# Kernel optimization log

Measured on AMD Instinct MI355X. Metric: run time of the kernel, lower is better.

The kernel has to match this reference:

```python
import jax, jax.numpy as jnp
import numpy as np

H = 128
N_USER, N_PC, N_URL = 100000, 20000, 50000
E_UP, E_UU = 250000, 500000
NUM_LAYERS = 2


def _sage(x_src, x_dst, src_idx, dst_idx, n_dst, Wl, bl, Wr):
    # PyG SAGEConv (aggr='mean', root_weight=True, lin_r bias=False):
    # out = lin_l(mean_j x_src[j]) + lin_r(x_dst)
    msg = x_src[src_idx]                                   # [E, H] gather
    agg = jax.ops.segment_sum(msg, dst_idx, num_segments=n_dst)
    cnt = jax.ops.segment_sum(jnp.ones((src_idx.shape[0], 1), x_src.dtype),
                              dst_idx, num_segments=n_dst)
    mean = agg / jnp.maximum(cnt, 1.0)
    return mean @ Wl + bl + x_dst @ Wr


def setup_inputs() -> dict:
    key = jax.random.key(0)
    ks = jax.random.split(key, 24)
    s = 0.05
    inp = {
        'x_user': jax.random.normal(ks[0], (N_USER, 6), jnp.float32),
        'x_pc': jax.random.normal(ks[1], (N_PC, 4), jnp.float32),
        'x_url': jax.random.normal(ks[2], (N_URL, 3), jnp.float32),
        'edge_up_src': jax.random.randint(ks[3], (E_UP,), 0, N_USER, jnp.int32),
        'edge_up_dst': jax.random.randint(ks[4], (E_UP,), 0, N_PC, jnp.int32),
        'edge_uu_src': jax.random.randint(ks[5], (E_UU,), 0, N_USER, jnp.int32),
        'edge_uu_dst': jax.random.randint(ks[6], (E_UU,), 0, N_URL, jnp.int32),
        # input projections
        'Wu': jax.random.normal(ks[7], (6, H), jnp.float32) * s,
        'bu': jnp.zeros((H,), jnp.float32),
        'Wp': jax.random.normal(ks[8], (4, H), jnp.float32) * s,
        'bp': jnp.zeros((H,), jnp.float32),
        'Wr_feat': jax.random.normal(ks[9], (3, H), jnp.float32) * s,
        'br_feat': jnp.zeros((H,), jnp.float32),
        # SAGEConv params, stacked over layers [L, H, H]
        'Wl_pc': jax.random.normal(ks[10], (NUM_LAYERS, H, H), jnp.float32) * s,
        'bl_pc': jnp.zeros((NUM_LAYERS, H), jnp.float32),
        'Wr_pc': jax.random.normal(ks[11], (NUM_LAYERS, H, H), jnp.float32) * s,
        'Wl_url': jax.random.normal(ks[12], (NUM_LAYERS, H, H), jnp.float32) * s,
        'bl_url': jnp.zeros((NUM_LAYERS, H), jnp.float32),
        'Wr_url': jax.random.normal(ks[13], (NUM_LAYERS, H, H), jnp.float32) * s,
        # context aggregation + classifier
        'Wctx': jax.random.normal(ks[14], (3 * H, H), jnp.float32) * s,
        'bctx': jnp.zeros((H,), jnp.float32),
        'Wc1': jax.random.normal(ks[15], (H, H // 2), jnp.float32) * s,
        'bc1': jnp.zeros((H // 2,), jnp.float32),
        'Wc2': jax.random.normal(ks[16], (H // 2, 2), jnp.float32) * s,
        'bc2': jnp.zeros((2,), jnp.float32),
    }
    return inp


def reference(x_user, x_pc, x_url,
              edge_up_src, edge_up_dst, edge_uu_src, edge_uu_dst,
              Wu, bu, Wp, bp, Wr_feat, br_feat,
              Wl_pc, bl_pc, Wr_pc, Wl_url, bl_url, Wr_url,
              Wctx, bctx, Wc1, bc1, Wc2, bc2):
    user = x_user @ Wu + bu          # [N_USER, H] (never updated by convs)
    pc = x_pc @ Wp + bp              # [N_PC, H]
    url = x_url @ Wr_feat + br_feat  # [N_URL, H]

    for i in range(NUM_LAYERS):
        pc_new = _sage(user, pc, edge_up_src, edge_up_dst, pc.shape[0],
                       Wl_pc[i], bl_pc[i], Wr_pc[i])
        url_new = _sage(user, url, edge_uu_src, edge_uu_dst, url.shape[0],
                        Wl_url[i], bl_url[i], Wr_url[i])
        if i == 0:
            pc = jax.nn.relu(pc_new)
            url = jax.nn.relu(url_new)
        else:
            pc = jax.nn.relu(pc_new + pc)
            url = jax.nn.relu(url_new + url)

    # aggregate_resource_context: scatter-add of resource embeddings into users
    pc_ctx = jax.ops.segment_sum(pc[edge_up_dst], edge_up_src, num_segments=user.shape[0])
    url_ctx = jax.ops.segment_sum(url[edge_uu_dst], edge_uu_src, num_segments=user.shape[0])
    combined = jnp.concatenate([user, pc_ctx, url_ctx], axis=1)   # [N_USER, 3H]
    enriched = combined @ Wctx + bctx

    # classifier (dropout inactive at inference)
    h = jax.nn.relu(enriched @ Wc1 + bc1)
    return h @ Wc2 + bc2
```

## Files before the change

### kernel.cpp

```cpp
#include <hip/hip_runtime.h>

typedef unsigned short u16;
typedef short short8_t __attribute__((ext_vector_type(8)));
typedef float floatx4 __attribute__((ext_vector_type(4)));

static constexpr int N_USER_C = 100000;
static constexpr int N_PC_C   = 20000;
static constexpr int N_URL_C  = 50000;
static constexpr int E_UP_C   = 250000;
static constexpr int E_UU_C   = 500000;

static constexpr int S_UPD = 48;
static constexpr int S_UUD = 40;
static constexpr int S_SRC = 24;

__device__ __forceinline__ float bf2f(u16 h) {
    return __uint_as_float(((unsigned)h) << 16);
}
__device__ __forceinline__ u16 f2bf(float f) {
    unsigned u = __float_as_uint(f);
    u += 0x7fffu + ((u >> 16) & 1u);
    return (u16)(u >> 16);
}

struct PFArgs {
    const float* wsrc[12];
    u16* wdst;
    const float *Xu, *Wu, *bu, *Xp, *Wp, *bp, *Xr, *Wr, *br;
    u16 *ou, *op, *orr;
    const int *up_src, *up_dst, *uu_src, *uu_dst;
    int *cnt_up_dst, *cnt_uu_dst, *cnt_up_src, *cnt_uu_src;
    int *val_up_dst, *val_uu_dst;
    u16 *val_up_src, *val_uu_src;
};
__global__ __launch_bounds__(256) void prepfill_kernel(PFArgs a)
{
    int b = blockIdx.x, tid = threadIdx.x;
    if (b < 1960) {
        const int range = b & 7;
        const int ebase = (b >> 3) * 2048 + tid;
#pragma unroll
        for (int i = 0; i < 8; ++i) {
            int e = ebase + i * 256;
            if (e < E_UP_C) {
                int s = __builtin_nontemporal_load(a.up_src + e);
                int d = __builtin_nontemporal_load(a.up_dst + e);
                if (d / 2500 == range) {
                    int p = atomicAdd(&a.cnt_up_dst[d], 1);
                    if (p < S_UPD) a.val_up_dst[d * S_UPD + p] = s;
                }
                if (s / 12500 == range) {
                    int p = atomicAdd(&a.cnt_up_src[s], 1);
                    if (p < S_SRC) a.val_up_src[s * S_SRC + p] = (u16)d;
                }
            }
            if (e < E_UU_C) {
                int s = __builtin_nontemporal_load(a.uu_src + e);
                int d = __builtin_nontemporal_load(a.uu_dst + e);
                if (d / 6250 == range) {
                    int p = atomicAdd(&a.cnt_uu_dst[d], 1);
                    if (p < S_UUD) a.val_uu_dst[d * S_UUD + p] = s;
                }
                if (s / 12500 == range) {
                    int p = atomicAdd(&a.cnt_uu_src[s], 1);
                    if (p < S_SRC) a.val_uu_src[s * S_SRC + p] = (u16)d;
                }
            }
        }
    } else if (b < 1960 + 768) {
        int idx = (b - 1960) * 256 + tid;
        int m = idx >> 14, e = idx & 16383;
        int n = e >> 7, k = e & 127;
        int Nm = (m == 11) ? 64 : 128;
        u16 v = 0;
        if (n < Nm) v = f2bf(a.wsrc[m][k * Nm + n]);
        a.wdst[(size_t)m * 16384 + n * 128 + k] = v;
    } else {
        int idx = (b - 1960 - 768) * 256 + tid;
        const float* X; const float* W; const float* bi; u16* o; int K;
        if (idx < 1600000)       { X = a.Xu; W = a.Wu; bi = a.bu; o = a.ou; K = 6; }
        else if (idx < 1920000)  { idx -= 1600000; X = a.Xp; W = a.Wp; bi = a.bp; o = a.op; K = 4; }
        else                     { idx -= 1920000; X = a.Xr; W = a.Wr; bi = a.br; o = a.orr; K = 3; }
        int r = idx >> 4, c0 = (idx & 15) * 8;
        float acc[8];
        {
            const float4 b0 = *(const float4*)(bi + c0);
            const float4 b1 = *(const float4*)(bi + c0 + 4);
            acc[0] = b0.x; acc[1] = b0.y; acc[2] = b0.z; acc[3] = b0.w;
            acc[4] = b1.x; acc[5] = b1.y; acc[6] = b1.z; acc[7] = b1.w;
        }
        for (int k = 0; k < K; ++k) {
            float xk = X[(size_t)r * K + k];
            const float4 w0 = *(const float4*)(W + k * 128 + c0);
            const float4 w1 = *(const float4*)(W + k * 128 + c0 + 4);
            acc[0] += xk * w0.x; acc[1] += xk * w0.y; acc[2] += xk * w0.z; acc[3] += xk * w0.w;
            acc[4] += xk * w1.x; acc[5] += xk * w1.y; acc[6] += xk * w1.z; acc[7] += xk * w1.w;
        }
        uint4 pk;
        pk.x = (unsigned)f2bf(acc[0]) | ((unsigned)f2bf(acc[1]) << 16);
        pk.y = (unsigned)f2bf(acc[2]) | ((unsigned)f2bf(acc[3]) << 16);
        pk.z = (unsigned)f2bf(acc[4]) | ((unsigned)f2bf(acc[5]) << 16);
        pk.w = (unsigned)f2bf(acc[6]) | ((unsigned)f2bf(acc[7]) << 16);
        *(uint4*)(o + (size_t)r * 128 + c0) = pk;
    }
}

__device__ __forceinline__ void gm_row(
    const u16* __restrict__ feat, const int* __restrict__ cnt,
    const int* __restrict__ vals, int stride, u16* __restrict__ outp, int row, int lane)
{
    int deg = cnt[row];
    deg = __builtin_amdgcn_readfirstlane(deg);
    int n = deg < stride ? deg : stride;
    const int* vp = vals + row * stride;
    float a0 = 0.f, a1 = 0.f, b0 = 0.f, b1 = 0.f;
    float c0 = 0.f, c1 = 0.f, d0 = 0.f, d1 = 0.f;
    int j = 0;
    for (; j + 4 <= n; j += 4) {
        int i0 = __builtin_nontemporal_load(vp + j);
        int i1 = __builtin_nontemporal_load(vp + j + 1);
        int i2 = __builtin_nontemporal_load(vp + j + 2);
        int i3 = __builtin_nontemporal_load(vp + j + 3);
        unsigned u0 = *(const unsigned*)(feat + (size_t)i0 * 128 + lane * 2);
        unsigned u1 = *(const unsigned*)(feat + (size_t)i1 * 128 + lane * 2);
        unsigned u2 = *(const unsigned*)(feat + (size_t)i2 * 128 + lane * 2);
        unsigned u3 = *(const unsigned*)(feat + (size_t)i3 * 128 + lane * 2);
        a0 += bf2f((u16)(u0 & 0xffff)); a1 += bf2f((u16)(u0 >> 16));
        b0 += bf2f((u16)(u1 & 0xffff)); b1 += bf2f((u16)(u1 >> 16));
        c0 += bf2f((u16)(u2 & 0xffff)); c1 += bf2f((u16)(u2 >> 16));
        d0 += bf2f((u16)(u3 & 0xffff)); d1 += bf2f((u16)(u3 >> 16));
    }
    for (; j < n; ++j) {
        int i0 = __builtin_nontemporal_load(vp + j);
        unsigned u0 = *(const unsigned*)(feat + (size_t)i0 * 128 + lane * 2);
        a0 += bf2f((u16)(u0 & 0xffff)); a1 += bf2f((u16)(u0 >> 16));
    }
    float ax = (a0 + b0) + (c0 + d0), ay = (a1 + b1) + (c1 + d1);
    float inv = 1.0f / fmaxf((float)deg, 1.0f);
    unsigned o = (unsigned)f2bf(ax * inv) | ((unsigned)f2bf(ay * inv) << 16);
    *(unsigned*)(outp + (size_t)row * 128 + lane * 2) = o;
}

__global__ __launch_bounds__(256) void gather_mean2_kernel(
    const u16* __restrict__ feat,
    const int* __restrict__ cnt_pc, const int* __restrict__ val_pc, u16* __restrict__ out_pc,
    const int* __restrict__ cnt_url, const int* __restrict__ val_url, u16* __restrict__ out_url)
{
    int b = blockIdx.x;
    int lane = threadIdx.x & 63, w = threadIdx.x >> 6;
    if (b < 5000) gm_row(feat, cnt_pc, val_pc, S_UPD, out_pc, b * 4 + w, lane);
    else          gm_row(feat, cnt_url, val_url, S_UUD, out_url, (b - 5000) * 4 + w, lane);
}

__device__ __forceinline__ unsigned ctx_ld(int t, int n0, const u16* __restrict__ vu,
    const u16* __restrict__ vr,
    const u16* __restrict__ pcW, const u16* __restrict__ urlW, int lane)
{
    bool isup = t < n0;
    const u16* vp = isup ? (vu + t) : (vr + (t - n0));
    int idx = __builtin_nontemporal_load(vp);
    const u16* base = isup ? pcW : urlW;
    return *(const unsigned*)(base + (size_t)idx * 128 + lane * 2);
}

__global__ __launch_bounds__(256) void ctx_gather_kernel(
    u16* __restrict__ enr,
    const int* __restrict__ cnt_up, const u16* __restrict__ val_up, const u16* __restrict__ pcW,
    const int* __restrict__ cnt_uu, const u16* __restrict__ val_uu, const u16* __restrict__ urlW,
    int M)
{
    int row = blockIdx.x * 4 + (threadIdx.x >> 6);
    if (row >= M) return;
    int lane = threadIdx.x & 63;
    int n0 = cnt_up[row], n1 = cnt_uu[row];
    n0 = __builtin_amdgcn_readfirstlane(n0); n1 = __builtin_amdgcn_readfirstlane(n1);
    n0 = n0 < S_SRC ? n0 : S_SRC; n1 = n1 < S_SRC ? n1 : S_SRC;
    int total = n0 + n1;
    const u16* vu = val_up + row * S_SRC;
    const u16* vr = val_uu + row * S_SRC;

    unsigned eu = *(const unsigned*)(enr + (size_t)row * 128 + lane * 2);
    float a0 = bf2f((u16)(eu & 0xffff)), a1 = bf2f((u16)(eu >> 16));
    float b0 = 0.f, b1 = 0.f, c0 = 0.f, c1 = 0.f, d0 = 0.f, d1 = 0.f;

    int t = 0;
    for (; t + 4 <= total; t += 4) {
        unsigned u0 = ctx_ld(t + 0, n0, vu, vr, pcW, urlW, lane);
        unsigned u1 = ctx_ld(t + 1, n0, vu, vr, pcW, urlW, lane);
        unsigned u2 = ctx_ld(t + 2, n0, vu, vr, pcW, urlW, lane);
        unsigned u3 = ctx_ld(t + 3, n0, vu, vr, pcW, urlW, lane);
        a0 += bf2f((u16)(u0 & 0xffff)); a1 += bf2f((u16)(u0 >> 16));
        b0 += bf2f((u16)(u1 & 0xffff)); b1 += bf2f((u16)(u1 >> 16));
        c0 += bf2f((u16)(u2 & 0xffff)); c1 += bf2f((u16)(u2 >> 16));
        d0 += bf2f((u16)(u3 & 0xffff)); d1 += bf2f((u16)(u3 >> 16));
    }
    for (; t < total; ++t) {
        unsigned u0 = ctx_ld(t, n0, vu, vr, pcW, urlW, lane);
        a0 += bf2f((u16)(u0 & 0xffff)); a1 += bf2f((u16)(u0 >> 16));
    }
    float ax = (a0 + b0) + (c0 + d0), ay = (a1 + b1) + (c1 + d1);
    unsigned o = (unsigned)f2bf(ax) | ((unsigned)f2bf(ay) << 16);
    *(unsigned*)(enr + (size_t)row * 128 + lane * 2) = o;
}

struct FSeg {
    const u16 *mean, *x0;
    const u16 *Wl0, *Wr0, *Wl1, *Wr1, *Wc;
    const float *b0, *b1;
    u16* out; int M; int bstart; int mode;
};
struct FArgs { FSeg s[3]; };

__global__ __launch_bounds__(256) void gemm_fused_kernel(FArgs fa)
{
    constexpr int XP = 136;
    __shared__ u16 Ws[2][128 * 40];
    __shared__ u16 Xs[128 * XP];

    int si = 0;
    if ((int)blockIdx.x >= fa.s[1].bstart) si = 1;
    if ((int)blockIdx.x >= fa.s[2].bstart) si = 2;
    FSeg sg = fa.s[si];
    const int bb = blockIdx.x - sg.bstart;

    const int tid = threadIdx.x;
    const int wave = tid >> 6, lane = tid & 63;
    const int m = lane & 15, kq = lane >> 4;
    const int rloc = wave * 32;
    const int rbase = bb * 128 + rloc;
    const int sn = tid >> 1, spart = tid & 1;

    floatx4 acc[2][8];

    auto zeroAcc = [&]() {
#pragma unroll
        for (int mt = 0; mt < 2; ++mt)
#pragma unroll
            for (int nt = 0; nt < 8; ++nt) acc[mt][nt] = (floatx4)0.0f;
    };
    auto stageW = [&](const u16* Wt, int kc, int buf) {
        *(short8_t*)&Ws[buf][sn * 40 + spart * 16] =
            *(const short8_t*)(Wt + (size_t)sn * 128 + kc + spart * 16);
        *(short8_t*)&Ws[buf][sn * 40 + spart * 16 + 8] =
            *(const short8_t*)(Wt + (size_t)sn * 128 + kc + spart * 16 + 8);
    };
    auto loadAg = [&](const u16* A, int kc, int mt) -> short8_t {
        int row = rbase + mt * 16 + m; row = row < sg.M ? row : sg.M - 1;
        return *(const short8_t*)(A + (size_t)row * 128 + kc + kq * 8);
    };
    auto loadAs = [&](int kc, int mt) -> short8_t {
        return *(const short8_t*)&Xs[(rloc + mt * 16 + m) * XP + kc + kq * 8];
    };
    auto mfmaChunk = [&](short8_t a0, short8_t a1, int buf) {
#pragma unroll
        for (int nt = 0; nt < 8; ++nt) {
            short8_t b = *(const short8_t*)&Ws[buf][(nt * 16 + m) * 40 + kq * 8];
            acc[0][nt] = __builtin_amdgcn_mfma_f32_16x16x32_bf16(a0, b, acc[0][nt], 0, 0, 0);
            acc[1][nt] = __builtin_amdgcn_mfma_f32_16x16x32_bf16(a1, b, acc[1][nt], 0, 0, 0);
        }
    };
    auto passDual = [&](const u16* W1, const u16* A1g, const u16* W2, const u16* A2g, bool a2lds) {
        zeroAcc();
        stageW(W1, 0, 0);
        short8_t an0 = loadAg(A1g, 0, 0), an1 = loadAg(A1g, 0, 1);
        __syncthreads();
        for (int c = 0; c < 8; ++c) {
            int c1 = c + 1;
            if (c1 < 8) {
                int kc1 = (c1 & 3) * 32;
                stageW(c1 < 4 ? W1 : W2, kc1, c1 & 1);
            }
            short8_t a0 = an0, a1 = an1;
            if (c1 < 8) {
                int kc1 = (c1 & 3) * 32;
                if (c1 < 4)     { an0 = loadAg(A1g, kc1, 0); an1 = loadAg(A1g, kc1, 1); }
                else if (a2lds) { an0 = loadAs(kc1, 0);      an1 = loadAs(kc1, 1); }
                else            { an0 = loadAg(A2g, kc1, 0); an1 = loadAg(A2g, kc1, 1); }
            }
            mfmaChunk(a0, a1, c & 1);
            __syncthreads();
        }
    };
    auto passSingle = [&](const u16* W1, const u16* A1g, bool lds) {
        zeroAcc();
        stageW(W1, 0, 0);
        short8_t an0, an1;
        if (lds) { an0 = loadAs(0, 0); an1 = loadAs(0, 1); }
        else     { an0 = loadAg(A1g, 0, 0); an1 = loadAg(A1g, 0, 1); }
        __syncthreads();
        for (int c = 0; c < 4; ++c) {
            int c1 = c + 1;
            if (c1 < 4) stageW(W1, c1 * 32, c1 & 1);
            short8_t a0 = an0, a1 = an1;
            if (c1 < 4) {
                if (lds) { an0 = loadAs(c1 * 32, 0); an1 = loadAs(c1 * 32, 1); }
                else     { an0 = loadAg(A1g, c1 * 32, 0); an1 = loadAg(A1g, c1 * 32, 1); }
            }
            mfmaChunk(a0, a1, c & 1);
            __syncthreads();
        }
    };
    auto epilogueToLds = [&](const float* bias, bool addRes) {
#pragma unroll
        for (int nt = 0; nt < 8; ++nt) {
            int col = nt * 16 + m;
            float bv = bias[col];
#pragma unroll
            for (int mt = 0; mt < 2; ++mt)
#pragma unroll
                for (int r = 0; r < 4; ++r) {
                    int lrow = rloc + mt * 16 + kq * 4 + r;
                    float v = acc[mt][nt][r] + bv;
                    if (addRes) v += bf2f(Xs[lrow * XP + col]);
                    Xs[lrow * XP + col] = f2bf(fmaxf(v, 0.f));
                }
        }
    };
    auto epilogueToGlobal = [&](const float* bias, u16* outp) {
#pragma unroll
        for (int nt = 0; nt < 8; ++nt) {
            int col = nt * 16 + m;
            float bv = bias ? bias[col] : 0.0f;
#pragma unroll
            for (int mt = 0; mt < 2; ++mt)
#pragma unroll
                for (int r = 0; r < 4; ++r) {
                    int row = rbase + mt * 16 + kq * 4 + r;
                    if (row < sg.M) outp[(size_t)row * 128 + col] = f2bf(acc[mt][nt][r] + bv);
                }
        }
    };

    if (sg.mode == 0) {
        passDual(sg.Wl0, sg.mean, sg.Wr0, sg.x0, false);
        epilogueToLds(sg.b0, false);
        passDual(sg.Wl1, sg.mean, sg.Wr1, nullptr, true);
        epilogueToLds(sg.b1, true);
        passSingle(sg.Wc, nullptr, true);
        epilogueToGlobal(nullptr, sg.out);
    } else {
        passSingle(sg.Wl0, sg.mean, false);
        epilogueToGlobal(sg.b0, sg.out);
    }
}

__global__ __launch_bounds__(256) void gemm_final_kernel(
    const u16* __restrict__ A1, const u16* __restrict__ Wt1,
    const float* __restrict__ bc1, const float* __restrict__ Wc2,
    const float* __restrict__ bc2, float* __restrict__ out, int M)
{
    constexpr int NT = 4;
    constexpr int PER_ROW = 4;
    constexpr int CHUNK = 8;
    constexpr int NC = 4;

    __shared__ u16 Ws[64 * 40];

    const int tid = threadIdx.x;
    const int wave = tid >> 6, lane = tid & 63;
    const int m = lane & 15, kq = lane >> 4;
    const int rbase = blockIdx.x * 128 + wave * 32;
    const int sn = tid / PER_ROW, spart = tid % PER_ROW;

    floatx4 acc[2][NT];
#pragma unroll
    for (int mt = 0; mt < 2; ++mt)
#pragma unroll
        for (int nt = 0; nt < NT; ++nt) acc[mt][nt] = (floatx4)0.0f;

    short8_t a_next[2];
#pragma unroll
    for (int mt = 0; mt < 2; ++mt) {
        int row = rbase + mt * 16 + m; row = row < M ? row : M - 1;
        a_next[mt] = *(const short8_t*)(A1 + (size_t)row * 128 + kq * 8);
    }

    for (int c = 0; c < NC; ++c) {
        __syncthreads();
        {
            short8_t v = *(const short8_t*)(Wt1 + (size_t)sn * 128 + c * 32 + spart * CHUNK);
            *(short8_t*)&Ws[sn * 40 + spart * CHUNK] = v;
        }
        short8_t a_cur[2] = { a_next[0], a_next[1] };
        __syncthreads();
        if (c + 1 < NC) {
            int kc1 = (c + 1) * 32;
#pragma unroll
            for (int mt = 0; mt < 2; ++mt) {
                int row = rbase + mt * 16 + m; row = row < M ? row : M - 1;
                a_next[mt] = *(const short8_t*)(A1 + (size_t)row * 128 + kc1 + kq * 8);
            }
        }
#pragma unroll
        for (int nt = 0; nt < NT; ++nt) {
            short8_t b = *(const short8_t*)&Ws[(nt * 16 + m) * 40 + kq * 8];
            acc[0][nt] = __builtin_amdgcn_mfma_f32_16x16x32_bf16(a_cur[0], b, acc[0][nt], 0, 0, 0);
            acc[1][nt] = __builtin_amdgcn_mfma_f32_16x16x32_bf16(a_cur[1], b, acc[1][nt], 0, 0, 0);
        }
    }

    float w0v[NT], w1v[NT], bv[NT];
#pragma unroll
    for (int nt = 0; nt < NT; ++nt) {
        int col = nt * 16 + m;
        w0v[nt] = Wc2[col * 2 + 0];
        w1v[nt] = Wc2[col * 2 + 1];
        bv[nt]  = bc1[col];
    }
    float b20 = bc2[0], b21 = bc2[1];

#pragma unroll
    for (int mt = 0; mt < 2; ++mt) {
#pragma unroll
        for (int r = 0; r < 4; ++r) {
            float o0 = 0.f, o1 = 0.f;
#pragma unroll
            for (int nt = 0; nt < NT; ++nt) {
                float v = acc[mt][nt][r] + bv[nt];
                v = fmaxf(v, 0.f);
                o0 += v * w0v[nt];
                o1 += v * w1v[nt];
            }
#pragma unroll
            for (int off = 1; off < 16; off <<= 1) {
                o0 += __shfl_xor(o0, off, 64);
                o1 += __shfl_xor(o1, off, 64);
            }
            if (m == 0) {
                int row = rbase + mt * 16 + kq * 4 + r;
                if (row < M) {
                    out[(size_t)row * 2 + 0] = o0 + b20;
                    out[(size_t)row * 2 + 1] = o1 + b21;
                }
            }
        }
    }
}

extern "C" void kernel_launch(void* const* d_in, const int* in_sizes, int n_in,
                              void* d_out, int out_size, void* d_ws, size_t ws_size,
                              hipStream_t stream)
{
    const float* x_user  = (const float*)d_in[0];
    const float* x_pc    = (const float*)d_in[1];
    const float* x_url   = (const float*)d_in[2];
    const int* e_up_src  = (const int*)d_in[3];
    const int* e_up_dst  = (const int*)d_in[4];
    const int* e_uu_src  = (const int*)d_in[5];
    const int* e_uu_dst  = (const int*)d_in[6];
    const float* Wu      = (const float*)d_in[7];
    const float* bu      = (const float*)d_in[8];
    const float* Wp      = (const float*)d_in[9];
    const float* bp      = (const float*)d_in[10];
    const float* Wr_feat = (const float*)d_in[11];
    const float* br_feat = (const float*)d_in[12];
    const float* Wl_pc   = (const float*)d_in[13];
    const float* bl_pc   = (const float*)d_in[14];
    const float* Wr_pc   = (const float*)d_in[15];
    const float* Wl_url  = (const float*)d_in[16];
    const float* bl_url  = (const float*)d_in[17];
    const float* Wr_url  = (const float*)d_in[18];
    const float* Wctx    = (const float*)d_in[19];
    const float* bctx    = (const float*)d_in[20];
    const float* Wc1     = (const float*)d_in[21];
    const float* bc1     = (const float*)d_in[22];
    const float* Wc2     = (const float*)d_in[23];
    const float* bc2     = (const float*)d_in[24];
    float* out = (float*)d_out;

    char* wsb = (char*)d_ws;
    u16* user_bf  = (u16*)(wsb);
    u16* enr      = (u16*)(wsb + 4ull *  6400000);
    u16* mean_pc  = (u16*)(wsb + 4ull * 12800000);
    u16* mean_url = (u16*)(wsb + 4ull * 14080000);
    u16* pc_a     = (u16*)(wsb + 4ull * 17280000);
    u16* pc_b     = (u16*)(wsb + 4ull * 18560000);
    u16* url_a    = (u16*)(wsb + 4ull * 19840000);
    u16* url_b    = (u16*)(wsb + 4ull * 23040000);
    u16* Wt       = (u16*)(wsb + 4ull * 26240000);
    int* cnts     = (int*)(wsb + 4ull * 26340000);
    int* up_dst_val = (int*)(wsb + 4ull * 26610000);
    int* uu_dst_val = (int*)(wsb + 4ull * 27570000);
    u16* up_src_val = (u16*)(wsb + 4ull * 29570000);
    u16* uu_src_val = (u16*)(wsb + 4ull * 30770000);

    int* cnt_up_dst = cnts + 0;
    int* cnt_uu_dst = cnts + 20000;
    int* cnt_up_src = cnts + 70000;
    int* cnt_uu_src = cnts + 170000;

    const int T = 256;

    hipMemsetAsync(cnts, 0, 270000ull * 4, stream);

    PFArgs pf;
    pf.wsrc[0] = Wl_pc;               pf.wsrc[1] = Wr_pc;
    pf.wsrc[2] = Wl_pc + 128 * 128;   pf.wsrc[3] = Wr_pc + 128 * 128;
    pf.wsrc[4] = Wl_url;              pf.wsrc[5] = Wr_url;
    pf.wsrc[6] = Wl_url + 128 * 128;  pf.wsrc[7] = Wr_url + 128 * 128;
    pf.wsrc[8] = Wctx;                pf.wsrc[9] = Wctx + 128 * 128;
    pf.wsrc[10] = Wctx + 256 * 128;   pf.wsrc[11] = Wc1;
    pf.wdst = Wt;
    pf.Xu = x_user; pf.Wu = Wu;      pf.bu = bu;      pf.ou = user_bf;
    pf.Xp = x_pc;   pf.Wp = Wp;      pf.bp = bp;      pf.op = pc_a;
    pf.Xr = x_url;  pf.Wr = Wr_feat; pf.br = br_feat; pf.orr = url_a;
    pf.up_src = e_up_src; pf.up_dst = e_up_dst;
    pf.uu_src = e_uu_src; pf.uu_dst = e_uu_dst;
    pf.cnt_up_dst = cnt_up_dst; pf.cnt_uu_dst = cnt_uu_dst;
    pf.cnt_up_src = cnt_up_src; pf.cnt_uu_src = cnt_uu_src;
    pf.val_up_dst = up_dst_val; pf.val_uu_dst = uu_dst_val;
    pf.val_up_src = up_src_val; pf.val_uu_src = uu_src_val;
    prepfill_kernel<<<1960 + 768 + 10625, T, 0, stream>>>(pf);

    gather_mean2_kernel<<<5000 + 12500, T, 0, stream>>>(
        user_bf, cnt_up_dst, up_dst_val, mean_pc, cnt_uu_dst, uu_dst_val, mean_url);

    FArgs fg;
    fg.s[0] = { mean_pc,  pc_a,  Wt + 0 * 16384, Wt + 1 * 16384, Wt + 2 * 16384, Wt + 3 * 16384,
                Wt + 9 * 16384,  bl_pc,  bl_pc + 128,  pc_b,  N_PC_C,   0,   0 };
    fg.s[1] = { mean_url, url_a, Wt + 4 * 16384, Wt + 5 * 16384, Wt + 6 * 16384, Wt + 7 * 16384,
                Wt + 10 * 16384, bl_url, bl_url + 128, url_b, N_URL_C,  157, 0 };
    fg.s[2] = { user_bf,  nullptr, Wt + 8 * 16384, nullptr, nullptr, nullptr,
                nullptr,         bctx,   nullptr,      enr,   N_USER_C, 548, 1 };
    gemm_fused_kernel<<<548 + 782, T, 0, stream>>>(fg);

    ctx_gather_kernel<<<(N_USER_C + 3) / 4, T, 0, stream>>>(
        enr, cnt_up_src, up_src_val, pc_b, cnt_uu_src, uu_src_val, url_b, N_USER_C);

    gemm_final_kernel<<<(N_USER_C + 127) / 128, T, 0, stream>>>(
        enr, Wt + 11 * 16384, bc1, Wc2, bc2, out, N_USER_C);
}
```

Before: 353.0 us.

## Fuse user ctx GEMM into gather kernel and ctx gather into final classifier

Moves the user-side Wctx projection GEMM out of the fused GEMM launch into the mean-gather launch as extra blocks, so the chain kernel only handles pc/url layers. Merges the context gather with the classifier GEMM: each block gathers 64 rows into LDS, then runs the Wc1 MFMA and the Wc2 reduction in place. This drops the enr round-trip and one launch. In exchange the final kernel stages the whole Wc1 into 64-row LDS tiles, and the gather runs serially per wave over 16 rows, which may reduce memory-level parallelism.

New measurement: 433.1 us. 22.7% more time.

```diff
diff --git a/kernel.cpp b/kernel.cpp
--- a/kernel.cpp
+++ b/kernel.cpp
@@ -141,85 +141,90 @@
     *(unsigned*)(outp + (size_t)row * 128 + lane * 2) = o;
 }
 
-__global__ __launch_bounds__(256) void gather_mean2_kernel(
+__global__ __launch_bounds__(256) void mean_ctx_kernel(
     const u16* __restrict__ feat,
     const int* __restrict__ cnt_pc, const int* __restrict__ val_pc, u16* __restrict__ out_pc,
-    const int* __restrict__ cnt_url, const int* __restrict__ val_url, u16* __restrict__ out_url)
+    const int* __restrict__ cnt_url, const int* __restrict__ val_url, u16* __restrict__ out_url,
+    const u16* __restrict__ Wctx_t, const float* __restrict__ bctx, u16* __restrict__ enr)
 {
-    int b = blockIdx.x;
-    int lane = threadIdx.x & 63, w = threadIdx.x >> 6;
-    if (b < 5000) gm_row(feat, cnt_pc, val_pc, S_UPD, out_pc, b * 4 + w, lane);
-    else          gm_row(feat, cnt_url, val_url, S_UUD, out_url, (b - 5000) * 4 + w, lane);
-}
-
-__device__ __forceinline__ unsigned ctx_ld(int t, int n0, const u16* __restrict__ vu,
-    const u16* __restrict__ vr,
-    const u16* __restrict__ pcW, const u16* __restrict__ urlW, int lane)
-{
-    bool isup = t < n0;
-    const u16* vp = isup ? (vu + t) : (vr + (t - n0));
-    int idx = __builtin_nontemporal_load(vp);
-    const u16* base = isup ? pcW : urlW;
-    return *(const unsigned*)(base + (size_t)idx * 128 + lane * 2);
-}
-
-__global__ __launch_bounds__(256) void ctx_gather_kernel(
-    u16* __restrict__ enr,
-    const int* __restrict__ cnt_up, const u16* __restrict__ val_up, const u16* __restrict__ pcW,
-    const int* __restrict__ cnt_uu, const u16* __restrict__ val_uu, const u16* __restrict__ urlW,
-    int M)
-{
-    int row = blockIdx.x * 4 + (threadIdx.x >> 6);
-    if (row >= M) return;
-    int lane = threadIdx.x & 63;
-    int n0 = cnt_up[row], n1 = cnt_uu[row];
-    n0 = __builtin_amdgcn_readfirstlane(n0); n1 = __builtin_amdgcn_readfirstlane(n1);
-    n0 = n0 < S_SRC ? n0 : S_SRC; n1 = n1 < S_SRC ? n1 : S_SRC;
-    int total = n0 + n1;
-    const u16* vu = val_up + row * S_SRC;
-    const u16* vr = val_uu + row * S_SRC;
-
-    unsigned eu = *(const unsigned*)(enr + (size_t)row * 128 + lane * 2);
-    float a0 = bf2f((u16)(eu & 0xffff)), a1 = bf2f((u16)(eu >> 16));
-    float b0 = 0.f, b1 = 0.f, c0 = 0.f, c1 = 0.f, d0 = 0.f, d1 = 0.f;
-
-    int t = 0;
-    for (; t + 4 <= total; t += 4) {
-        unsigned u0 = ctx_ld(t + 0, n0, vu, vr, pcW, urlW, lane);
-        unsigned u1 = ctx_ld(t + 1, n0, vu, vr, pcW, urlW, lane);
-        unsigned u2 = ctx_ld(t + 2, n0, vu, vr, pcW, urlW, lane);
-        unsigned u3 = ctx_ld(t + 3, n0, vu, vr, pcW, urlW, lane);
-        a0 += bf2f((u16)(u0 & 0xffff)); a1 += bf2f((u16)(u0 >> 16));
-        b0 += bf2f((u16)(u1 & 0xffff)); b1 += bf2f((u16)(u1 >> 16));
-        c0 += bf2f((u16)(u2 & 0xffff)); c1 += bf2f((u16)(u2 >> 16));
-        d0 += bf2f((u16)(u3 & 0xffff)); d1 += bf2f((u16)(u3 >> 16));
-    }
-    for (; t < total; ++t) {
-        unsigned u0 = ctx_ld(t, n0, vu, vr, pcW, urlW, lane);
-        a0 += bf2f((u16)(u0 & 0xffff)); a1 += bf2f((u16)(u0 >> 16));
-    }
-    float ax = (a0 + b0) + (c0 + d0), ay = (a1 + b1) + (c1 + d1);
-    unsigned o = (unsigned)f2bf(ax) | ((unsigned)f2bf(ay) << 16);
-    *(unsigned*)(enr + (size_t)row * 128 + lane * 2) = o;
+    __shared__ u16 Ws[2][128 * 40];
+    const int b = blockIdx.x, tid = threadIdx.x;
+    const int wave = tid >> 6, lane = tid & 63;
+
+    if (b >= 782) {
+        int bg = b - 782;
+        if (bg < 5000) gm_row(feat, cnt_pc, val_pc, S_UPD, out_pc, bg * 4 + wave, lane);
+        else           gm_row(feat, cnt_url, val_url, S_UUD, out_url, (bg - 5000) * 4 + wave, lane);
+        return;
+    }
+
+    const int m = lane & 15, kq = lane >> 4;
+    const int rbase = b * 128 + wave * 32;
+    const int sn = tid >> 1, spart = tid & 1;
+    const int M = N_USER_C;
+
+    floatx4 acc[2][8];
+#pragma unroll
+    for (int mt = 0; mt < 2; ++mt)
+#pragma unroll
+        for (int nt = 0; nt < 8; ++nt) acc[mt][nt] = (floatx4)0.0f;
+
+    auto stageW = [&](int kc, int buf) {
+        *(short8_t*)&Ws[buf][sn * 40 + spart * 16] =
+            *(const short8_t*)(Wctx_t + (size_t)sn * 128 + kc + spart * 16);
+        *(short8_t*)&Ws[buf][sn * 40 + spart * 16 + 8] =
+            *(const short8_t*)(Wctx_t + (size_t)sn * 128 + kc + spart * 16 + 8);
+    };
+    auto loadA = [&](int kc, int mt) -> short8_t {
+        int row = rbase + mt * 16 + m; row = row < M ? row : M - 1;
+        return *(const short8_t*)(feat + (size_t)row * 128 + kc + kq * 8);
+    };
+
+    stageW(0, 0);
+    short8_t an0 = loadA(0, 0), an1 = loadA(0, 1);
+    __syncthreads();
+    for (int c = 0; c < 4; ++c) {
+        int c1 = c + 1;
+        if (c1 < 4) stageW(c1 * 32, c1 & 1);
+        short8_t a0 = an0, a1 = an1;
+        if (c1 < 4) { an0 = loadA(c1 * 32, 0); an1 = loadA(c1 * 32, 1); }
+#pragma unroll
+        for (int nt = 0; nt < 8; ++nt) {
+            short8_t bb = *(const short8_t*)&Ws[c & 1][(nt * 16 + m) * 40 + kq * 8];
+            acc[0][nt] = __builtin_amdgcn_mfma_f32_16x16x32_bf16(a0, bb, acc[0][nt], 0, 0, 0);
+            acc[1][nt] = __builtin_amdgcn_mfma_f32_16x16x32_bf16(a1, bb, acc[1][nt], 0, 0, 0);
+        }
+        __syncthreads();
+    }
+#pragma unroll
+    for (int nt = 0; nt < 8; ++nt) {
+        int col = nt * 16 + m;
+        float bv = bctx[col];
+#pragma unroll
+        for (int mt = 0; mt < 2; ++mt)
+#pragma unroll
+            for (int r = 0; r < 4; ++r) {
+                int row = rbase + mt * 16 + kq * 4 + r;
+                if (row < M) enr[(size_t)row * 128 + col] = f2bf(acc[mt][nt][r] + bv);
+            }
+    }
 }
 
 struct FSeg {
     const u16 *mean, *x0;
     const u16 *Wl0, *Wr0, *Wl1, *Wr1, *Wc;
     const float *b0, *b1;
-    u16* out; int M; int bstart; int mode;
+    u16* out; int M; int bstart;
 };
-struct FArgs { FSeg s[3]; };
-
-__global__ __launch_bounds__(256) void gemm_fused_kernel(FArgs fa)
+struct FArgs { FSeg s[2]; };
+
+__global__ __launch_bounds__(256) void chain_kernel(FArgs fa)
 {
     constexpr int XP = 136;
     __shared__ u16 Ws[2][128 * 40];
     __shared__ u16 Xs[128 * XP];
 
-    int si = 0;
-    if ((int)blockIdx.x >= fa.s[1].bstart) si = 1;
-    if ((int)blockIdx.x >= fa.s[2].bstart) si = 2;
+    int si = ((int)blockIdx.x >= fa.s[1].bstart) ? 1 : 0;
     FSeg sg = fa.s[si];
     const int bb = blockIdx.x - sg.bstart;
 
@@ -281,21 +286,16 @@
             __syncthreads();
         }
     };
-    auto passSingle = [&](const u16* W1, const u16* A1g, bool lds) {
+    auto passSingleLds = [&](const u16* W1) {
         zeroAcc();
         stageW(W1, 0, 0);
-        short8_t an0, an1;
-        if (lds) { an0 = loadAs(0, 0); an1 = loadAs(0, 1); }
-        else     { an0 = loadAg(A1g, 0, 0); an1 = loadAg(A1g, 0, 1); }
+        short8_t an0 = loadAs(0, 0), an1 = loadAs(0, 1);
         __syncthreads();
         for (int c = 0; c < 4; ++c) {
             int c1 = c + 1;
             if (c1 < 4) stageW(W1, c1 * 32, c1 & 1);
             short8_t a0 = an0, a1 = an1;
-            if (c1 < 4) {
-                if (lds) { an0 = loadAs(c1 * 32, 0); an1 = loadAs(c1 * 32, 1); }
-                else     { an0 = loadAg(A1g, c1 * 32, 0); an1 = loadAg(A1g, c1 * 32, 1); }
-            }
+            if (c1 < 4) { an0 = loadAs(c1 * 32, 0); an1 = loadAs(c1 * 32, 1); }
             mfmaChunk(a0, a1, c & 1);
             __syncthreads();
         }
@@ -315,123 +315,134 @@
                     Xs[lrow * XP + col] = f2bf(fmaxf(v, 0.f));
                 }
         }
-    };
-    auto epilogueToGlobal = [&](const float* bias, u16* outp) {
+        __syncthreads();
+    };
+    auto epilogueToGlobal = [&](u16* outp) {
 #pragma unroll
         for (int nt = 0; nt < 8; ++nt) {
             int col = nt * 16 + m;
-            float bv = bias ? bias[col] : 0.0f;
 #pragma unroll
             for (int mt = 0; mt < 2; ++mt)
 #pragma unroll
                 for (int r = 0; r < 4; ++r) {
                     int row = rbase + mt * 16 + kq * 4 + r;
-                    if (row < sg.M) outp[(size_t)row * 128 + col] = f2bf(acc[mt][nt][r] + bv);
+                    if (row < sg.M) outp[(size_t)row * 128 + col] = f2bf(acc[mt][nt][r]);
                 }
         }
     };
 
-    if (sg.mode == 0) {
-        passDual(sg.Wl0, sg.mean, sg.Wr0, sg.x0, false);
-        epilogueToLds(sg.b0, false);
-        passDual(sg.Wl1, sg.mean, sg.Wr1, nullptr, true);
-        epilogueToLds(sg.b1, true);
-        passSingle(sg.Wc, nullptr, true);
-        epilogueToGlobal(nullptr, sg.out);
-    } else {
-        passSingle(sg.Wl0, sg.mean, false);
-        epilogueToGlobal(sg.b0, sg.out);
-    }
-}
-
-__global__ __launch_bounds__(256) void gemm_final_kernel(
-    const u16* __restrict__ A1, const u16* __restrict__ Wt1,
-    const float* __restrict__ bc1, const float* __restrict__ Wc2,
-    const float* __restrict__ bc2, float* __restrict__ out, int M)
+    passDual(sg.Wl0, sg.mean, sg.Wr0, sg.x0, false);
+    epilogueToLds(sg.b0, false);
+    passDual(sg.Wl1, sg.mean, sg.Wr1, nullptr, true);
+    epilogueToLds(sg.b1, true);
+    passSingleLds(sg.Wc);
+    epilogueToGlobal(sg.out);
+}
+
+__global__ __launch_bounds__(256) void ctx_final_kernel(
+    const u16* __restrict__ enr,
+    const int* __restrict__ cnt_up, const u16* __restrict__ val_up, const u16* __restrict__ pcW,
+    const int* __restrict__ cnt_uu, const u16* __restrict__ val_uu, const u16* __restrict__ urlW,
+    const u16* __restrict__ Wc1_t, const float* __restrict__ bc1,
+    const float* __restrict__ Wc2, const float* __restrict__ bc2,
+    float* __restrict__ out, int M)
 {
-    constexpr int NT = 4;
-    constexpr int PER_ROW = 4;
-    constexpr int CHUNK = 8;
-    constexpr int NC = 4;
-
-    __shared__ u16 Ws[64 * 40];
+    __shared__ u16 Xs[64 * 136];
+    __shared__ u16 Wc1s[64 * 136];
 
     const int tid = threadIdx.x;
     const int wave = tid >> 6, lane = tid & 63;
     const int m = lane & 15, kq = lane >> 4;
-    const int rbase = blockIdx.x * 128 + wave * 32;
-    const int sn = tid / PER_ROW, spart = tid % PER_ROW;
-
-    floatx4 acc[2][NT];
-#pragma unroll
-    for (int mt = 0; mt < 2; ++mt)
-#pragma unroll
-        for (int nt = 0; nt < NT; ++nt) acc[mt][nt] = (floatx4)0.0f;
-
-    short8_t a_next[2];
-#pragma unroll
-    for (int mt = 0; mt < 2; ++mt) {
-        int row = rbase + mt * 16 + m; row = row < M ? row : M - 1;
-        a_next[mt] = *(const short8_t*)(A1 + (size_t)row * 128 + kq * 8);
-    }
-
-    for (int c = 0; c < NC; ++c) {
-        __syncthreads();
-        {
-            short8_t v = *(const short8_t*)(Wt1 + (size_t)sn * 128 + c * 32 + spart * CHUNK);
-            *(short8_t*)&Ws[sn * 40 + spart * CHUNK] = v;
-        }
-        short8_t a_cur[2] = { a_next[0], a_next[1] };
-        __syncthreads();
-        if (c + 1 < NC) {
-            int kc1 = (c + 1) * 32;
-#pragma unroll
-            for (int mt = 0; mt < 2; ++mt) {
-                int row = rbase + mt * 16 + m; row = row < M ? row : M - 1;
-                a_next[mt] = *(const short8_t*)(A1 + (size_t)row * 128 + kc1 + kq * 8);
-            }
-        }
-#pragma unroll
-        for (int nt = 0; nt < NT; ++nt) {
-            short8_t b = *(const short8_t*)&Ws[(nt * 16 + m) * 40 + kq * 8];
-            acc[0][nt] = __builtin_amdgcn_mfma_f32_16x16x32_bf16(a_cur[0], b, acc[0][nt], 0, 0, 0);
-            acc[1][nt] = __builtin_amdgcn_mfma_f32_16x16x32_bf16(a_cur[1], b, acc[1][nt], 0, 0, 0);
-        }
-    }
-
-    float w0v[NT], w1v[NT], bv[NT];
-#pragma unroll
-    for (int nt = 0; nt < NT; ++nt) {
+    const int rbw = blockIdx.x * 64 + wave * 16;
+
+    for (int idx = tid; idx < 64 * 16; idx += 256) {
+        int row = idx >> 4, part = idx & 15;
+        *(short8_t*)&Wc1s[row * 136 + part * 8] =
+            *(const short8_t*)(Wc1_t + (size_t)row * 128 + part * 8);
+    }
+
+    for (int rr = 0; rr < 16; ++rr) {
+        int row = rbw + rr;
+        int lrow = wave * 16 + rr;
+        unsigned o = 0;
+        if (row < M) {
+            int n0 = cnt_up[row], n1 = cnt_uu[row];
+            n0 = __builtin_amdgcn_readfirstlane(n0); n1 = __builtin_amdgcn_readfirstlane(n1);
+            n0 = n0 < S_SRC ? n0 : S_SRC; n1 = n1 < S_SRC ? n1 : S_SRC;
+            int total = n0 + n1;
+            const u16* vu = val_up + row * S_SRC;
+            const u16* vr = val_uu + row * S_SRC;
+            unsigned eu = *(const unsigned*)(enr + (size_t)row * 128 + lane * 2);
+            float a0 = bf2f((u16)(eu & 0xffff)), a1 = bf2f((u16)(eu >> 16));
+            float b0 = 0.f, b1 = 0.f, c0 = 0.f, c1 = 0.f, d0 = 0.f, d1 = 0.f;
+            auto ld = [&](int t) -> unsigned {
+                bool isup = t < n0;
+                int idx = isup ? vu[t] : vr[t - n0];
+                const u16* base = isup ? pcW : urlW;
+                return *(const unsigned*)(base + (size_t)idx * 128 + lane * 2);
+            };
+            int t = 0;
+            for (; t + 4 <= total; t += 4) {
+                unsigned u0 = ld(t + 0), u1 = ld(t + 1), u2 = ld(t + 2), u3 = ld(t + 3);
+                a0 += bf2f((u16)(u0 & 0xffff)); a1 += bf2f((u16)(u0 >> 16));
+                b0 += bf2f((u16)(u1 & 0xffff)); b1 += bf2f((u16)(u1 >> 16));
+                c0 += bf2f((u16)(u2 & 0xffff)); c1 += bf2f((u16)(u2 >> 16));
+                d0 += bf2f((u16)(u3 & 0xffff)); d1 += bf2f((u16)(u3 >> 16));
+            }
+            for (; t < total; ++t) {
+                unsigned u0 = ld(t);
+                a0 += bf2f((u16)(u0 & 0xffff)); a1 += bf2f((u16)(u0 >> 16));
+            }
+            float ax = (a0 + b0) + (c0 + d0), ay = (a1 + b1) + (c1 + d1);
+            o = (unsigned)f2bf(ax) | ((unsigned)f2bf(ay) << 16);
+        }
+        *(unsigned*)&Xs[lrow * 136 + 2 * lane] = o;
+    }
+
+    __syncthreads();
+
+    floatx4 acc2[4];
+#pragma unroll
+    for (int nt = 0; nt < 4; ++nt) acc2[nt] = (floatx4)0.0f;
+    for (int c = 0; c < 4; ++c) {
+        int kc = c * 32;
+        short8_t a = *(const short8_t*)&Xs[(wave * 16 + m) * 136 + kc + kq * 8];
+#pragma unroll
+        for (int nt = 0; nt < 4; ++nt) {
+            short8_t b = *(const short8_t*)&Wc1s[(nt * 16 + m) * 136 + kc + kq * 8];
+            acc2[nt] = __builtin_amdgcn_mfma_f32_16x16x32_bf16(a, b, acc2[nt], 0, 0, 0);
+        }
+    }
+
+    float w0v[4], w1v[4], bv[4];
+#pragma unroll
+    for (int nt = 0; nt < 4; ++nt) {
         int col = nt * 16 + m;
         w0v[nt] = Wc2[col * 2 + 0];
         w1v[nt] = Wc2[col * 2 + 1];
         bv[nt]  = bc1[col];
     }
     float b20 = bc2[0], b21 = bc2[1];
-
-#pragma unroll
-    for (int mt = 0; mt < 2; ++mt) {
-#pragma unroll
-        for (int r = 0; r < 4; ++r) {
-            float o0 = 0.f, o1 = 0.f;
-#pragma unroll
-            for (int nt = 0; nt < NT; ++nt) {
-                float v = acc[mt][nt][r] + bv[nt];
-                v = fmaxf(v, 0.f);
-                o0 += v * w0v[nt];
-                o1 += v * w1v[nt];
-            }
-#pragma unroll
-            for (int off = 1; off < 16; off <<= 1) {
-                o0 += __shfl_xor(o0, off, 64);
-                o1 += __shfl_xor(o1, off, 64);
-            }
-            if (m == 0) {
-                int row = rbase + mt * 16 + kq * 4 + r;
-                if (row < M) {
-                    out[(size_t)row * 2 + 0] = o0 + b20;
-                    out[(size_t)row * 2 + 1] = o1 + b21;
-                }
+#pragma unroll
+    for (int r = 0; r < 4; ++r) {
+        float o0 = 0.f, o1 = 0.f;
+#pragma unroll
+        for (int nt = 0; nt < 4; ++nt) {
+            float v = acc2[nt][r] + bv[nt];
+            v = fmaxf(v, 0.f);
+            o0 += v * w0v[nt];
+            o1 += v * w1v[nt];
+        }
+#pragma unroll
+        for (int off = 1; off < 16; off <<= 1) {
+            o0 += __shfl_xor(o0, off, 64);
+            o1 += __shfl_xor(o1, off, 64);
+        }
+        if (m == 0) {
+            int row = rbw + kq * 4 + r;
+            if (row < M) {
+                out[(size_t)row * 2 + 0] = o0 + b20;
+                out[(size_t)row * 2 + 1] = o1 + b21;
             }
         }
     }
@@ -512,21 +523,18 @@
     pf.val_up_src = up_src_val; pf.val_uu_src = uu_src_val;
     prepfill_kernel<<<1960 + 768 + 10625, T, 0, stream>>>(pf);
 
-    gather_mean2_kernel<<<5000 + 12500, T, 0, stream>>>(
-        user_bf, cnt_up_dst, up_dst_val, mean_pc, cnt_uu_dst, uu_dst_val, mean_url);
+    mean_ctx_kernel<<<782 + 17500, T, 0, stream>>>(
+        user_bf, cnt_up_dst, up_dst_val, mean_pc, cnt_uu_dst, uu_dst_val, mean_url,
+        Wt + 8 * 16384, bctx, enr);
 
     FArgs fg;
     fg.s[0] = { mean_pc,  pc_a,  Wt + 0 * 16384, Wt + 1 * 16384, Wt + 2 * 16384, Wt + 3 * 16384,
-                Wt + 9 * 16384,  bl_pc,  bl_pc + 128,  pc_b,  N_PC_C,   0,   0 };
+                Wt + 9 * 16384,  bl_pc,  bl_pc + 128,  pc_b,  N_PC_C,   0 };
     fg.s[1] = { mean_url, url_a, Wt + 4 * 16384, Wt + 5 * 16384, Wt + 6 * 16384, Wt + 7 * 16384,
-                Wt + 10 * 16384, bl_url, bl_url + 128, url_b, N_URL_C,  157, 0 };
-    fg.s[2] = { user_bf,  nullptr, Wt + 8 * 16384, nullptr, nullptr, nullptr,
-                nullptr,         bctx,   nullptr,      enr,   N_USER_C, 548, 1 };
-    gemm_fused_kernel<<<548 + 782, T, 0, stream>>>(fg);
-
-    ctx_gather_kernel<<<(N_USER_C + 3) / 4, T, 0, stream>>>(
-        enr, cnt_up_src, up_src_val, pc_b, cnt_uu_src, uu_src_val, url_b, N_USER_C);
-
-    gemm_final_kernel<<<(N_USER_C + 127) / 128, T, 0, stream>>>(
-        enr, Wt + 11 * 16384, bc1, Wc2, bc2, out, N_USER_C);
-}
+                Wt + 10 * 16384, bl_url, bl_url + 128, url_b, N_URL_C,  157 };
+    chain_kernel<<<548, T, 0, stream>>>(fg);
+
+    ctx_final_kernel<<<(N_USER_C + 63) / 64, T, 0, stream>>>(
+        enr, cnt_up_src, up_src_val, pc_b, cnt_uu_src, uu_src_val, url_b,
+        Wt + 11 * 16384, bc1, Wc2, bc2, out, N_USER_C);
+}
```
